# Kernel tuning notes

Measured on AMD Instinct MI355X. Metric: run time of the kernel, lower is better.

The kernel has to match this reference:

```python
import jax, jax.numpy as jnp
import numpy as np

N = 100000   # nodes
G = 256      # graphs
E = 120000   # edges per relation
IN = 162
HID = 128
R = 5
L = 2        # extra RGCN layers beyond the initial one


def setup_inputs() -> dict:
    key = jax.random.key(0)
    ks = jax.random.split(key, 24)
    s = 0.05
    inp = {
        "X": jax.random.normal(ks[0], (N, IN), jnp.float32),
        "batch": jnp.sort(jax.random.randint(ks[6], (N,), 0, G)),
    }
    for i in range(R):
        inp[f"edge_index{i+1}"] = jax.random.randint(ks[1 + i], (2, E), 0, N)
    # RGCN initial layer params
    inp["W0"] = jax.random.normal(ks[7], (R, IN, HID), jnp.float32) * s
    inp["root0"] = jax.random.normal(ks[8], (IN, HID), jnp.float32) * s
    inp["b0"] = jnp.zeros((HID,), jnp.float32)
    # stacked params for the L hidden RGCN layers
    inp["Wl"] = jax.random.normal(ks[9], (L, R, HID, HID), jnp.float32) * s
    inp["rootl"] = jax.random.normal(ks[10], (L, HID, HID), jnp.float32) * s
    inp["bl"] = jnp.zeros((L, HID), jnp.float32)
    # classification head
    inp["Wc1"] = jax.random.normal(ks[11], (HID, HID), jnp.float32) * s
    inp["bc1"] = jnp.zeros((HID,), jnp.float32)
    inp["Wc2"] = jax.random.normal(ks[12], (HID, HID), jnp.float32) * s
    inp["bc2"] = jnp.zeros((HID,), jnp.float32)
    inp["Wc3"] = jax.random.normal(ks[13], (HID, 1), jnp.float32) * s
    inp["bc3"] = jnp.zeros((1,), jnp.float32)
    return inp


def _seg_mean(msg, dst, num):
    # scatter-mean over destination nodes (PyG RGCNConv uses aggr='mean' per relation)
    s = jax.ops.segment_sum(msg, dst, num_segments=num)
    c = jax.ops.segment_sum(jnp.ones(msg.shape[0], msg.dtype), dst, num_segments=num)
    return s / jnp.maximum(c, 1.0)[:, None]


def _rgcn(x, W, root, b, src, dst):
    # src, dst: [R, E]; W: [R, d_in, d_out]
    msgs = jnp.einsum("ref,rfh->reh", x[src], W)          # [R, E, HID]
    agg = jax.vmap(_seg_mean, in_axes=(0, 0, None))(msgs, dst, N)  # [R, N, HID]
    return x @ root + b + agg.sum(0)


def reference(X, edge_index1, edge_index2, edge_index3, edge_index4, edge_index5,
              batch, W0, root0, b0, Wl, rootl, bl, Wc1, bc1, Wc2, bc2, Wc3, bc3):
    ei = jnp.stack([edge_index1, edge_index2, edge_index3, edge_index4, edge_index5])  # [R,2,E]
    src, dst = ei[:, 0, :], ei[:, 1, :]
    h = jax.nn.relu(_rgcn(X, W0, root0, b0, src, dst))
    for l in range(L):
        h = jax.nn.relu(_rgcn(h, Wl[l], rootl[l], bl[l], src, dst))
    # mean readout over graphs
    s = jax.ops.segment_sum(h, batch, num_segments=G)
    c = jax.ops.segment_sum(jnp.ones((N,), h.dtype), batch, num_segments=G)
    read = s / jnp.maximum(c, 1.0)[:, None]
    h = jax.nn.relu(read @ Wc1 + bc1)
    h = jax.nn.relu(h @ Wc2 + bc2)
    return h @ Wc3 + bc3
```

## Files before the change

### kernel.cpp

```cpp
#include <hip/hip_runtime.h>

#define N_NODES 100000
#define NPAD    100096
#define G_GRAPHS 256
#define IN_F 162
#define KPAD0 192
#define HID 128
#define R_REL 5
#define L_LAYERS 2
#define M5 (R_REL * N_NODES)

typedef __attribute__((ext_vector_type(8))) short bf16x8;
typedef __attribute__((ext_vector_type(4))) float f32x4;

__device__ __forceinline__ short f2bf(float f) {
    union { float f; unsigned u; } v; v.f = f;
    unsigned r = (v.u + 0x7fffu + ((v.u >> 16) & 1u)) >> 16;
    return (short)r;
}
__device__ __forceinline__ float bf2f(unsigned short u) {
    union { unsigned u; float f; } v; v.u = ((unsigned)u) << 16;
    return v.f;
}

__global__ void k_count(const int* e0, const int* e1, const int* e2,
                        const int* e3, const int* e4, int* cnt, int E) {
    int gid = blockIdx.x * 256 + threadIdx.x;
    if (gid >= R_REL * E) return;
    int r = gid / E, e = gid - r * E;
    const int* ei = (r == 0) ? e0 : (r == 1) ? e1 : (r == 2) ? e2 : (r == 3) ? e3 : e4;
    atomicAdd(&cnt[r * N_NODES + ei[E + e]], 1);
}

__global__ __launch_bounds__(256) void k_scan1(const int* __restrict__ cnt,
                                               int* __restrict__ off, int* __restrict__ bsum) {
    __shared__ int ts[256];
    int t = threadIdx.x;
    int base = blockIdx.x * 1024 + t * 4;
    int v[4];
    #pragma unroll
    for (int j = 0; j < 4; j++) {
        int d = base + j;
        int s = 0;
        if (d < N_NODES) {
            #pragma unroll
            for (int r = 0; r < R_REL; r++) s += cnt[r * N_NODES + d];
        }
        v[j] = s;
    }
    int tsum = v[0] + v[1] + v[2] + v[3];
    ts[t] = tsum; __syncthreads();
    for (int o = 1; o < 256; o <<= 1) {
        int x = (t >= o) ? ts[t - o] : 0;
        __syncthreads();
        ts[t] += x;
        __syncthreads();
    }
    if (t == 255) bsum[blockIdx.x] = ts[255];
    int run = ts[t] - tsum;
    #pragma unroll
    for (int j = 0; j < 4; j++) { if (base + j < N_NODES) off[base + j] = run; run += v[j]; }
}

__global__ __launch_bounds__(512) void k_scan2(int* bsum, int nblk) {
    __shared__ int ts[512];
    int t = threadIdx.x;
    int v = (t < nblk) ? bsum[t] : 0;
    ts[t] = v; __syncthreads();
    for (int o = 1; o < 512; o <<= 1) {
        int x = (t >= o) ? ts[t - o] : 0;
        __syncthreads();
        ts[t] += x;
        __syncthreads();
    }
    if (t < nblk) bsum[t] = ts[t] - v;
}

__global__ void k_scan3(const int* __restrict__ off, const int* __restrict__ bsum,
                        int* __restrict__ mstart, int* __restrict__ mcur,
                        const int* __restrict__ cnt, float* __restrict__ invc) {
    int i = blockIdx.x * 256 + threadIdx.x;
    if (i >= N_NODES) return;
    int o = off[i] + bsum[i >> 10];
    mstart[i] = o;
    mcur[i] = o;
    int tc = 0;
    #pragma unroll
    for (int r = 0; r < R_REL; r++) {
        int c = cnt[r * N_NODES + i];
        tc += c;
        invc[r * N_NODES + i] = 1.0f / (float)max(c, 1);
    }
    if (i == N_NODES - 1) mstart[N_NODES] = o + tc;
}

__global__ void k_fill(const int* e0, const int* e1, const int* e2,
                       const int* e3, const int* e4, int* mcur,
                       const float* __restrict__ invc,
                       int* __restrict__ mrec, float* __restrict__ mw, int E) {
    int gid = blockIdx.x * 256 + threadIdx.x;
    if (gid >= R_REL * E) return;
    int r = gid / E, e = gid - r * E;
    const int* ei = (r == 0) ? e0 : (r == 1) ? e1 : (r == 2) ? e2 : (r == 3) ? e3 : e4;
    int src = ei[e], dst = ei[E + e];
    int pos = atomicAdd(&mcur[dst], 1);
    mrec[pos] = ((1 + r) * NPAD + src) * HID;
    mw[pos] = invc[r * N_NODES + dst];
}

__global__ void k_tw0(const float* __restrict__ root0, const float* __restrict__ W0,
                      short* __restrict__ out) {
    int gid = blockIdx.x * 256 + threadIdx.x;
    if (gid >= 6 * 128 * KPAD0) return;
    int chunk = gid / (128 * KPAD0);
    int rem = gid - chunk * 128 * KPAD0;
    int col = rem / KPAD0;
    int k = rem - col * KPAD0;
    float v = 0.f;
    if (k < IN_F)
        v = (chunk == 0) ? root0[k * HID + col]
                         : W0[((size_t)(chunk - 1) * IN_F + k) * HID + col];
    out[gid] = f2bf(v);
}

__global__ void k_twl(const float* __restrict__ rootl, const float* __restrict__ Wl,
                      short* __restrict__ out) {
    int gid = blockIdx.x * 256 + threadIdx.x;
    if (gid >= L_LAYERS * 6 * 128 * HID) return;
    int l = gid / (6 * 128 * HID);
    int rem = gid - l * 6 * 128 * HID;
    int chunk = rem / (128 * HID);
    int rem2 = rem - chunk * 128 * HID;
    int col = rem2 / HID;
    int k = rem2 - col * HID;
    float v = (chunk == 0) ? rootl[((size_t)l * HID + k) * HID + col]
                           : Wl[(((size_t)l * R_REL + (chunk - 1)) * HID + k) * HID + col];
    out[gid] = f2bf(v);
}

template<int KP, bool A_F32>
__global__ __launch_bounds__(256, 2)
void gemm_fused(const void* __restrict__ Av, const short* __restrict__ Wt,
                unsigned short* __restrict__ Y, int M, int Kreal) {
    constexpr int SA = KP + 8;
    constexpr int NC8 = KP / 8;
    __shared__ short As[128 * SA];
    __shared__ short Bs[128 * SA];
    const int tid = threadIdx.x;
    const int row0 = blockIdx.x * 128;
    const int lane = tid & 63, wv = tid >> 6;
    const int quad = lane >> 4, l16 = lane & 15;
    const int wr0 = (wv >> 1) * 64, wc0 = (wv & 1) * 64;

    for (int cidx = tid; cidx < 128 * NC8; cidx += 256) {
        int row = cidx / NC8, c8 = cidx - row * NC8;
        int grow = row0 + row, k = c8 * 8;
        bf16x8 v = (bf16x8){0,0,0,0,0,0,0,0};
        if (grow < M) {
            if (A_F32) {
                const float* Af = (const float*)Av;
                #pragma unroll
                for (int j = 0; j < 8; j++) {
                    int kk = k + j;
                    float f = (kk < Kreal) ? Af[(size_t)grow * Kreal + kk] : 0.f;
                    v[j] = f2bf(f);
                }
            } else {
                v = *(const bf16x8*)((const short*)Av + (size_t)grow * KP + k);
            }
        }
        *(bf16x8*)&As[row * SA + k] = v;
    }

    for (int chunk = 0; chunk < 6; chunk++) {
        __syncthreads();
        const short* Wc = Wt + (size_t)chunk * 128 * KP;
        for (int cidx = tid; cidx < 128 * NC8; cidx += 256) {
            int row = cidx / NC8, c8 = cidx - row * NC8;
            *(bf16x8*)&Bs[row * SA + c8 * 8] = *(const bf16x8*)&Wc[row * KP + c8 * 8];
        }
        __syncthreads();

        f32x4 acc[4][4];
        #pragma unroll
        for (int i = 0; i < 4; i++)
            #pragma unroll
            for (int j = 0; j < 4; j++) acc[i][j] = (f32x4){0.f, 0.f, 0.f, 0.f};

        #pragma unroll
        for (int ks = 0; ks < KP / 32; ks++) {
            int k0 = ks * 32;
            bf16x8 af[4], bfr[4];
            #pragma unroll
            for (int i = 0; i < 4; i++)
                af[i] = *(const bf16x8*)&As[(wr0 + i * 16 + l16) * SA + k0 + quad * 8];
            #pragma unroll
            for (int j = 0; j < 4; j++)
                bfr[j] = *(const bf16x8*)&Bs[(wc0 + j * 16 + l16) * SA + k0 + quad * 8];
            #pragma unroll
            for (int i = 0; i < 4; i++)
                #pragma unroll
                for (int j = 0; j < 4; j++)
                    acc[i][j] = __builtin_amdgcn_mfma_f32_16x16x32_bf16(af[i], bfr[j], acc[i][j], 0, 0, 0);
        }
        __syncthreads();

        #pragma unroll
        for (int i = 0; i < 4; i++)
            #pragma unroll
            for (int j = 0; j < 4; j++)
                #pragma unroll
                for (int reg = 0; reg < 4; reg++)
                    Bs[(wr0 + i * 16 + quad * 4 + reg) * SA + wc0 + j * 16 + l16] =
                        f2bf(acc[i][j][reg]);
        __syncthreads();

        unsigned short* Yc = Y + (size_t)chunk * NPAD * HID + (size_t)row0 * HID;
        #pragma unroll
        for (int s = 0; s < 8; s++) {
            int row = (tid >> 4) + s * 16;
            int col = (tid & 15) * 8;
            bf16x8 v = *(const bf16x8*)&Bs[row * SA + col];
            *(bf16x8*)&Yc[(size_t)row * HID + col] = v;
        }
    }
}

__global__ __launch_bounds__(256)
void aggregate(const unsigned short* __restrict__ Yall, const int* __restrict__ mstart,
               const int* __restrict__ mrec, const float* __restrict__ mw,
               const float* __restrict__ bias, unsigned short* __restrict__ hout) {
    int wid = (blockIdx.x * 256 + threadIdx.x) >> 6;
    int lane = threadIdx.x & 63;
    if (wid >= N_NODES) return;
    int d = wid;
    int s = mstart[d], e = mstart[d + 1];

    float2 b2 = *(const float2*)&bias[lane * 2];
    unsigned rv = *(const unsigned*)&Yall[(size_t)d * HID + lane * 2];
    float s0 = b2.x + bf2f((unsigned short)(rv & 0xffff));
    float s1 = b2.y + bf2f((unsigned short)(rv >> 16));

    for (int base = s; base < e; base += 64) {
        int m = e - base;
        int rec = 0; float w = 0.f;
        if (lane < m) { rec = mrec[base + lane]; w = mw[base + lane]; }
        int cnt = min(m, 64);
        for (int j = 0; j < cnt; j++) {
            int off = __shfl(rec, j, 64);
            float wj = __shfl(w, j, 64);
            unsigned v = *(const unsigned*)&Yall[(size_t)off + lane * 2];
            s0 += wj * bf2f((unsigned short)(v & 0xffff));
            s1 += wj * bf2f((unsigned short)(v >> 16));
        }
    }
    unsigned lo = (unsigned short)f2bf(fmaxf(s0, 0.f));
    unsigned hi = (unsigned short)f2bf(fmaxf(s1, 0.f));
    *(unsigned*)&hout[(size_t)d * HID + lane * 2] = lo | (hi << 16);
}

__global__ __launch_bounds__(128)
void k_pool(const unsigned short* __restrict__ h, const int* __restrict__ batch,
            float* __restrict__ pooled) {
    int c = threadIdx.x;
    int start = blockIdx.x * 128;
    if (start >= N_NODES) return;
    int end = min(start + 128, N_NODES);
    int g = batch[start];
    float s = 0.f;
    for (int i = start; i < end; i++) {
        int gi = batch[i];
        if (gi != g) { atomicAdd(&pooled[g * HID + c], s); s = 0.f; g = gi; }
        s += bf2f(h[(size_t)i * HID + c]);
    }
    atomicAdd(&pooled[g * HID + c], s);
}

__device__ int lower_bound_i(const int* a, int n, int v) {
    int lo = 0, hi = n;
    while (lo < hi) {
        int mid = (lo + hi) >> 1;
        if (a[mid] < v) lo = mid + 1; else hi = mid;
    }
    return lo;
}

__global__ __launch_bounds__(128)
void k_mlp(const float* __restrict__ pooled, const int* __restrict__ batch,
           const float* __restrict__ Wc1, const float* __restrict__ bc1,
           const float* __restrict__ Wc2, const float* __restrict__ bc2,
           const float* __restrict__ Wc3, const float* __restrict__ bc3,
           float* __restrict__ out) {
    int g = blockIdx.x;
    int c = threadIdx.x;
    __shared__ int range[2];
    if (c == 0) range[0] = lower_bound_i(batch, N_NODES, g);
    if (c == 1) range[1] = lower_bound_i(batch, N_NODES, g + 1);
    __syncthreads();
    float denom = fmaxf((float)(range[1] - range[0]), 1.0f);
    __shared__ float row[HID], h1[HID], h2[HID];
    row[c] = pooled[g * HID + c] / denom;
    __syncthreads();
    float acc = bc1[c];
    for (int k = 0; k < HID; k++) acc += row[k] * Wc1[k * HID + c];
    h1[c] = fmaxf(acc, 0.f);
    __syncthreads();
    acc = bc2[c];
    for (int k = 0; k < HID; k++) acc += h1[k] * Wc2[k * HID + c];
    h2[c] = fmaxf(acc, 0.f);
    __syncthreads();
    float t = h2[c] * Wc3[c];
    for (int off = 32; off > 0; off >>= 1) t += __shfl_down(t, off, 64);
    __shared__ float part[2];
    if ((c & 63) == 0) part[c >> 6] = t;
    __syncthreads();
    if (c == 0) out[g] = part[0] + part[1] + bc3[0];
}

extern "C" void kernel_launch(void* const* d_in, const int* in_sizes, int n_in,
                              void* d_out, int out_size, void* d_ws, size_t ws_size,
                              hipStream_t stream) {
    const float* X     = (const float*)d_in[0];
    const int*   batch = (const int*)d_in[1];
    const int*   e0 = (const int*)d_in[2];
    const int*   e1 = (const int*)d_in[3];
    const int*   e2 = (const int*)d_in[4];
    const int*   e3 = (const int*)d_in[5];
    const int*   e4 = (const int*)d_in[6];
    const float* W0    = (const float*)d_in[7];
    const float* root0 = (const float*)d_in[8];
    const float* b0    = (const float*)d_in[9];
    const float* Wl    = (const float*)d_in[10];
    const float* rootl = (const float*)d_in[11];
    const float* bl    = (const float*)d_in[12];
    const float* Wc1   = (const float*)d_in[13];
    const float* bc1   = (const float*)d_in[14];
    const float* Wc2   = (const float*)d_in[15];
    const float* bc2   = (const float*)d_in[16];
    const float* Wc3   = (const float*)d_in[17];
    const float* bc3   = (const float*)d_in[18];
    const int E = in_sizes[2] / 2;
    const int NE = R_REL * E;

    char* base = (char*)d_ws;
    size_t o = 0;
    auto carve = [&](size_t bytes) -> char* {
        char* p = base + o;
        o = (o + bytes + 255) & ~(size_t)255;
        return p;
    };
    unsigned short* Y    = (unsigned short*)carve((size_t)6 * NPAD * HID * 2);
    unsigned short* hA   = (unsigned short*)carve((size_t)NPAD * HID * 2);
    unsigned short* hB   = (unsigned short*)carve((size_t)NPAD * HID * 2);
    int*   cnt    = (int*)carve((size_t)M5 * 4);
    float* invc   = (float*)carve((size_t)M5 * 4);
    int*   offsc  = (int*)carve((size_t)N_NODES * 4);
    int*   mstart = (int*)carve((size_t)(N_NODES + 1) * 4);
    int*   mcur   = (int*)carve((size_t)N_NODES * 4);
    int*   mrec   = (int*)carve((size_t)NE * 4);
    float* mw     = (float*)carve((size_t)NE * 4);
    int*   bsum   = (int*)carve(2048);
    float* pooled = (float*)carve((size_t)G_GRAPHS * HID * 4);
    short* Wt0    = (short*)carve((size_t)6 * 128 * KPAD0 * 2);
    short* Wtl    = (short*)carve((size_t)L_LAYERS * 6 * 128 * HID * 2);

    hipMemsetAsync(cnt, 0, (size_t)M5 * 4, stream);
    hipMemsetAsync(pooled, 0, (size_t)G_GRAPHS * HID * 4, stream);
    int eg = (NE + 255) / 256;
    k_count<<<eg, 256, 0, stream>>>(e0, e1, e2, e3, e4, cnt, E);
    int nblk = (N_NODES + 1023) / 1024;
    k_scan1<<<nblk, 256, 0, stream>>>(cnt, offsc, bsum);
    k_scan2<<<1, 512, 0, stream>>>(bsum, nblk);
    k_scan3<<<(N_NODES + 255) / 256, 256, 0, stream>>>(offsc, bsum, mstart, mcur, cnt, invc);
    k_fill<<<eg, 256, 0, stream>>>(e0, e1, e2, e3, e4, mcur, invc, mrec, mw, E);

    k_tw0<<<(6 * 128 * KPAD0 + 255) / 256, 256, 0, stream>>>(root0, W0, Wt0);
    k_twl<<<(L_LAYERS * 6 * 128 * HID + 255) / 256, 256, 0, stream>>>(rootl, Wl, Wtl);

    int ggrid = NPAD / 128;
    int agg_grid = (N_NODES + 3) / 4;

    gemm_fused<KPAD0, true><<<ggrid, 256, 0, stream>>>(X, Wt0, Y, N_NODES, IN_F);
    aggregate<<<agg_grid, 256, 0, stream>>>(Y, mstart, mrec, mw, b0, hA);

    unsigned short* hin = hA; unsigned short* hout = hB;
    for (int l = 0; l < L_LAYERS; l++) {
        gemm_fused<HID, false><<<ggrid, 256, 0, stream>>>(hin, Wtl + (size_t)l * 6 * 128 * HID,
                                                          Y, N_NODES, HID);
        aggregate<<<agg_grid, 256, 0, stream>>>(Y, mstart, mrec, mw, bl + (size_t)l * HID, hout);
        unsigned short* t = hin; hin = hout; hout = t;
    }

    k_pool<<<(N_NODES + 127) / 128, 128, 0, stream>>>(hin, batch, pooled);
    k_mlp<<<G_GRAPHS, 128, 0, stream>>>(pooled, batch, Wc1, bc1, Wc2, bc2, Wc3, bc3, (float*)d_out);
}
```

Measured before the change: 718.8 us.

## Split GEMM across output chunks with direct register A loads and XCD-aware tiling

Replaces the GEMM that staged the A tile in LDS and looped over six weight chunks inside one block. Each block now computes a single chunk, so the grid is six times larger, and it reads A fragments straight from global memory into registers with prefetching. Block IDs are remapped so the row tiles that share A land on the same XCD, aiming for L2 reuse. X is pre-cast to padded bf16 by a new kernel. The cost is reading A six times from global or L2 memory plus an extra cast pass over X.

```diff
diff --git a/kernel.cpp b/kernel.cpp
--- a/kernel.cpp
+++ b/kernel.cpp
@@ -2,6 +2,8 @@
 
 #define N_NODES 100000
 #define NPAD    100096
+#define NTILES  782
+#define TPX     98
 #define G_GRAPHS 256
 #define IN_F 162
 #define KPAD0 192
@@ -106,6 +108,14 @@
     int pos = atomicAdd(&mcur[dst], 1);
     mrec[pos] = ((1 + r) * NPAD + src) * HID;
     mw[pos] = invc[r * N_NODES + dst];
+}
+
+__global__ void k_castX(const float* __restrict__ X, unsigned short* __restrict__ Xb) {
+    int gid = blockIdx.x * 256 + threadIdx.x;
+    if (gid >= NPAD * KPAD0) return;
+    int row = gid / KPAD0, k = gid - row * KPAD0;
+    float v = (row < N_NODES && k < IN_F) ? X[(size_t)row * IN_F + k] : 0.f;
+    Xb[gid] = (unsigned short)f2bf(v);
 }
 
 __global__ void k_tw0(const float* __restrict__ root0, const float* __restrict__ W0,
@@ -138,62 +148,61 @@
     out[gid] = f2bf(v);
 }
 
-template<int KP, bool A_F32>
-__global__ __launch_bounds__(256, 2)
-void gemm_fused(const void* __restrict__ Av, const short* __restrict__ Wt,
-                unsigned short* __restrict__ Y, int M, int Kreal) {
+template<int KP>
+__global__ __launch_bounds__(256)
+void gemm_direct(const unsigned short* __restrict__ A, const short* __restrict__ Wt,
+                 unsigned short* __restrict__ Y) {
+    constexpr int KS = KP / 32;
+    constexpr int PF = (KS > 4) ? 2 : KS;
     constexpr int SA = KP + 8;
-    constexpr int NC8 = KP / 8;
-    __shared__ short As[128 * SA];
     __shared__ short Bs[128 * SA];
+
+    int bid = blockIdx.x;
+    int xcd = bid & 7, slot = bid >> 3;
+    int chunk = slot / TPX;
+    int rt = xcd * TPX + (slot - chunk * TPX);
+    if (rt >= NTILES) return;
+    const int row0 = rt * 128;
+
     const int tid = threadIdx.x;
-    const int row0 = blockIdx.x * 128;
     const int lane = tid & 63, wv = tid >> 6;
     const int quad = lane >> 4, l16 = lane & 15;
     const int wr0 = (wv >> 1) * 64, wc0 = (wv & 1) * 64;
 
-    for (int cidx = tid; cidx < 128 * NC8; cidx += 256) {
-        int row = cidx / NC8, c8 = cidx - row * NC8;
-        int grow = row0 + row, k = c8 * 8;
-        bf16x8 v = (bf16x8){0,0,0,0,0,0,0,0};
-        if (grow < M) {
-            if (A_F32) {
-                const float* Af = (const float*)Av;
-                #pragma unroll
-                for (int j = 0; j < 8; j++) {
-                    int kk = k + j;
-                    float f = (kk < Kreal) ? Af[(size_t)grow * Kreal + kk] : 0.f;
-                    v[j] = f2bf(f);
-                }
-            } else {
-                v = *(const bf16x8*)((const short*)Av + (size_t)grow * KP + k);
-            }
-        }
-        *(bf16x8*)&As[row * SA + k] = v;
-    }
-
-    for (int chunk = 0; chunk < 6; chunk++) {
-        __syncthreads();
-        const short* Wc = Wt + (size_t)chunk * 128 * KP;
-        for (int cidx = tid; cidx < 128 * NC8; cidx += 256) {
-            int row = cidx / NC8, c8 = cidx - row * NC8;
-            *(bf16x8*)&Bs[row * SA + c8 * 8] = *(const bf16x8*)&Wc[row * KP + c8 * 8];
-        }
-        __syncthreads();
-
-        f32x4 acc[4][4];
+    const size_t arow = (size_t)(row0 + wr0 + l16) * KP + quad * 8;
+
+    bf16x8 cur[PF][4], nxt[PF][4];
+    #pragma unroll
+    for (int p = 0; p < PF; p++)
         #pragma unroll
         for (int i = 0; i < 4; i++)
-            #pragma unroll
-            for (int j = 0; j < 4; j++) acc[i][j] = (f32x4){0.f, 0.f, 0.f, 0.f};
-
+            cur[p][i] = *(const bf16x8*)&A[arow + (size_t)i * 16 * KP + p * 32];
+
+    const short* Wc = Wt + (size_t)chunk * 128 * KP;
+    for (int cidx = tid; cidx < 128 * (KP / 8); cidx += 256) {
+        int row = cidx / (KP / 8), c8 = cidx - row * (KP / 8);
+        *(bf16x8*)&Bs[row * SA + c8 * 8] = *(const bf16x8*)&Wc[row * KP + c8 * 8];
+    }
+    __syncthreads();
+
+    f32x4 acc[4][4];
+    #pragma unroll
+    for (int i = 0; i < 4; i++)
         #pragma unroll
-        for (int ks = 0; ks < KP / 32; ks++) {
-            int k0 = ks * 32;
-            bf16x8 af[4], bfr[4];
-            #pragma unroll
-            for (int i = 0; i < 4; i++)
-                af[i] = *(const bf16x8*)&As[(wr0 + i * 16 + l16) * SA + k0 + quad * 8];
+        for (int j = 0; j < 4; j++) acc[i][j] = (f32x4){0.f, 0.f, 0.f, 0.f};
+
+    for (int kb = 0; kb < KS; kb += PF) {
+        if (kb + PF < KS) {
+            #pragma unroll
+            for (int p = 0; p < PF; p++)
+                #pragma unroll
+                for (int i = 0; i < 4; i++)
+                    nxt[p][i] = *(const bf16x8*)&A[arow + (size_t)i * 16 * KP + (kb + PF + p) * 32];
+        }
+        #pragma unroll
+        for (int p = 0; p < PF; p++) {
+            int k0 = (kb + p) * 32;
+            bf16x8 bfr[4];
             #pragma unroll
             for (int j = 0; j < 4; j++)
                 bfr[j] = *(const bf16x8*)&Bs[(wc0 + j * 16 + l16) * SA + k0 + quad * 8];
@@ -201,28 +210,33 @@
             for (int i = 0; i < 4; i++)
                 #pragma unroll
                 for (int j = 0; j < 4; j++)
-                    acc[i][j] = __builtin_amdgcn_mfma_f32_16x16x32_bf16(af[i], bfr[j], acc[i][j], 0, 0, 0);
+                    acc[i][j] = __builtin_amdgcn_mfma_f32_16x16x32_bf16(cur[p][i], bfr[j], acc[i][j], 0, 0, 0);
         }
-        __syncthreads();
-
         #pragma unroll
-        for (int i = 0; i < 4; i++)
-            #pragma unroll
-            for (int j = 0; j < 4; j++)
-                #pragma unroll
-                for (int reg = 0; reg < 4; reg++)
-                    Bs[(wr0 + i * 16 + quad * 4 + reg) * SA + wc0 + j * 16 + l16] =
-                        f2bf(acc[i][j][reg]);
-        __syncthreads();
-
-        unsigned short* Yc = Y + (size_t)chunk * NPAD * HID + (size_t)row0 * HID;
+        for (int p = 0; p < PF; p++)
+            #pragma unroll
+            for (int i = 0; i < 4; i++)
+                cur[p][i] = nxt[p][i];
+    }
+    __syncthreads();
+
+    #pragma unroll
+    for (int i = 0; i < 4; i++)
         #pragma unroll
-        for (int s = 0; s < 8; s++) {
-            int row = (tid >> 4) + s * 16;
-            int col = (tid & 15) * 8;
-            bf16x8 v = *(const bf16x8*)&Bs[row * SA + col];
-            *(bf16x8*)&Yc[(size_t)row * HID + col] = v;
-        }
+        for (int j = 0; j < 4; j++)
+            #pragma unroll
+            for (int reg = 0; reg < 4; reg++)
+                Bs[(wr0 + i * 16 + quad * 4 + reg) * SA + wc0 + j * 16 + l16] =
+                    f2bf(acc[i][j][reg]);
+    __syncthreads();
+
+    unsigned short* Yc = Y + (size_t)chunk * NPAD * HID + (size_t)row0 * HID;
+    #pragma unroll
+    for (int s = 0; s < 8; s++) {
+        int row = (tid >> 4) + s * 16;
+        int col = (tid & 15) * 8;
+        bf16x8 v = *(const bf16x8*)&Bs[row * SA + col];
+        *(bf16x8*)&Yc[(size_t)row * HID + col] = v;
     }
 }
 
@@ -352,6 +366,7 @@
     unsigned short* Y    = (unsigned short*)carve((size_t)6 * NPAD * HID * 2);
     unsigned short* hA   = (unsigned short*)carve((size_t)NPAD * HID * 2);
     unsigned short* hB   = (unsigned short*)carve((size_t)NPAD * HID * 2);
+    unsigned short* Xb   = (unsigned short*)carve((size_t)NPAD * KPAD0 * 2);
     int*   cnt    = (int*)carve((size_t)M5 * 4);
     float* invc   = (float*)carve((size_t)M5 * 4);
     int*   offsc  = (int*)carve((size_t)N_NODES * 4);
@@ -373,20 +388,19 @@
     k_scan2<<<1, 512, 0, stream>>>(bsum, nblk);
     k_scan3<<<(N_NODES + 255) / 256, 256, 0, stream>>>(offsc, bsum, mstart, mcur, cnt, invc);
     k_fill<<<eg, 256, 0, stream>>>(e0, e1, e2, e3, e4, mcur, invc, mrec, mw, E);
-
+    k_castX<<<(NPAD * KPAD0 + 255) / 256, 256, 0, stream>>>(X, Xb);
     k_tw0<<<(6 * 128 * KPAD0 + 255) / 256, 256, 0, stream>>>(root0, W0, Wt0);
     k_twl<<<(L_LAYERS * 6 * 128 * HID + 255) / 256, 256, 0, stream>>>(rootl, Wl, Wtl);
 
-    int ggrid = NPAD / 128;
+    int ggrid = 8 * TPX * 6;
     int agg_grid = (N_NODES + 3) / 4;
 
-    gemm_fused<KPAD0, true><<<ggrid, 256, 0, stream>>>(X, Wt0, Y, N_NODES, IN_F);
+    gemm_direct<KPAD0><<<ggrid, 256, 0, stream>>>(Xb, Wt0, Y);
     aggregate<<<agg_grid, 256, 0, stream>>>(Y, mstart, mrec, mw, b0, hA);
 
     unsigned short* hin = hA; unsigned short* hout = hB;
     for (int l = 0; l < L_LAYERS; l++) {
-        gemm_fused<HID, false><<<ggrid, 256, 0, stream>>>(hin, Wtl + (size_t)l * 6 * 128 * HID,
-                                                          Y, N_NODES, HID);
+        gemm_direct<HID><<<ggrid, 256, 0, stream>>>(hin, Wtl + (size_t)l * 6 * 128 * HID, Y);
         aggregate<<<agg_grid, 256, 0, stream>>>(Y, mstart, mrec, mw, bl + (size_t)l * HID, hout);
         unsigned short* t = hin; hin = hout; hout = t;
     }
```

Measured after the change: 693.3 us. -3.5%, faster.

## Keep GEMM A-tile in registers and batch gather loads in aggregate

Applied to the files above, without the earlier changes.

The GEMM kernel no longer stages the A tile in shared memory. Each wave loads its A fragments straight from global memory into registers once and reuses them across all six weight chunks, which cuts LDS use and raises occupancy for the hidden layers. The aggregate kernel now issues up to eight independent gather loads before accumulating, so more memory requests are in flight. The trade-off is higher register pressure: the first layer holds 24 bf16x8 fragments per thread. The A loads are also uncoalesced direct fragment loads.

```diff
diff --git a/kernel.cpp b/kernel.cpp
--- a/kernel.cpp
+++ b/kernel.cpp
@@ -2,6 +2,7 @@
 
 #define N_NODES 100000
 #define NPAD    100096
+#define NTILES  782
 #define G_GRAPHS 256
 #define IN_F 162
 #define KPAD0 192
@@ -138,46 +139,62 @@
     out[gid] = f2bf(v);
 }
 
-template<int KP, bool A_F32>
-__global__ __launch_bounds__(256, 2)
-void gemm_fused(const void* __restrict__ Av, const short* __restrict__ Wt,
-                unsigned short* __restrict__ Y, int M, int Kreal) {
-    constexpr int SA = KP + 8;
-    constexpr int NC8 = KP / 8;
-    __shared__ short As[128 * SA];
-    __shared__ short Bs[128 * SA];
+template<int SEG, bool A_F32, int MINW>
+__global__ __launch_bounds__(256, MINW)
+void gemm_reg(const void* __restrict__ Av, const short* __restrict__ Wt,
+              unsigned short* __restrict__ Y) {
+    constexpr int KSEG = SEG / 32;
+    constexpr int SBP = SEG + 8;
+    __shared__ short Bs[128 * SBP];
     const int tid = threadIdx.x;
     const int row0 = blockIdx.x * 128;
     const int lane = tid & 63, wv = tid >> 6;
     const int quad = lane >> 4, l16 = lane & 15;
     const int wr0 = (wv >> 1) * 64, wc0 = (wv & 1) * 64;
 
-    for (int cidx = tid; cidx < 128 * NC8; cidx += 256) {
-        int row = cidx / NC8, c8 = cidx - row * NC8;
-        int grow = row0 + row, k = c8 * 8;
-        bf16x8 v = (bf16x8){0,0,0,0,0,0,0,0};
-        if (grow < M) {
-            if (A_F32) {
-                const float* Af = (const float*)Av;
-                #pragma unroll
-                for (int j = 0; j < 8; j++) {
-                    int kk = k + j;
-                    float f = (kk < Kreal) ? Af[(size_t)grow * Kreal + kk] : 0.f;
-                    v[j] = f2bf(f);
+    bf16x8 af[KSEG][4];
+    #pragma unroll
+    for (int i = 0; i < 4; i++) {
+        int grow = row0 + wr0 + i * 16 + l16;
+        if (A_F32) {
+            const float* rp = (const float*)Av + (size_t)grow * IN_F;
+            bool ok = grow < N_NODES;
+            #pragma unroll
+            for (int kb = 0; kb < KSEG; kb++) {
+                bf16x8 v;
+                if (kb < 5) {
+                    int k = kb * 32 + quad * 8;
+                    #pragma unroll
+                    for (int h = 0; h < 4; h++) {
+                        float2 f2 = ok ? *(const float2*)(rp + k + 2 * h)
+                                       : make_float2(0.f, 0.f);
+                        v[2 * h] = f2bf(f2.x); v[2 * h + 1] = f2bf(f2.y);
+                    }
+                } else {
+                    int k = 160 + quad * 8;
+                    #pragma unroll
+                    for (int j = 0; j < 8; j++) {
+                        int kk = k + j;
+                        float f = (ok && kk < IN_F) ? rp[kk] : 0.f;
+                        v[j] = f2bf(f);
+                    }
                 }
-            } else {
-                v = *(const bf16x8*)((const short*)Av + (size_t)grow * KP + k);
+                af[kb][i] = v;
             }
-        }
-        *(bf16x8*)&As[row * SA + k] = v;
+        } else {
+            const unsigned short* Ab = (const unsigned short*)Av;
+            #pragma unroll
+            for (int kb = 0; kb < KSEG; kb++)
+                af[kb][i] = *(const bf16x8*)&Ab[(size_t)grow * SEG + kb * 32 + quad * 8];
+        }
     }
 
     for (int chunk = 0; chunk < 6; chunk++) {
-        __syncthreads();
-        const short* Wc = Wt + (size_t)chunk * 128 * KP;
-        for (int cidx = tid; cidx < 128 * NC8; cidx += 256) {
-            int row = cidx / NC8, c8 = cidx - row * NC8;
-            *(bf16x8*)&Bs[row * SA + c8 * 8] = *(const bf16x8*)&Wc[row * KP + c8 * 8];
+        if (chunk) __syncthreads();
+        const short* Wc = Wt + (size_t)chunk * 128 * SEG;
+        for (int c = tid; c < 128 * (SEG / 8); c += 256) {
+            int r = c / (SEG / 8), c8 = (c - r * (SEG / 8)) * 8;
+            *(bf16x8*)&Bs[r * SBP + c8] = *(const bf16x8*)&Wc[r * SEG + c8];
         }
         __syncthreads();
 
@@ -188,20 +205,16 @@
             for (int j = 0; j < 4; j++) acc[i][j] = (f32x4){0.f, 0.f, 0.f, 0.f};
 
         #pragma unroll
-        for (int ks = 0; ks < KP / 32; ks++) {
-            int k0 = ks * 32;
-            bf16x8 af[4], bfr[4];
-            #pragma unroll
-            for (int i = 0; i < 4; i++)
-                af[i] = *(const bf16x8*)&As[(wr0 + i * 16 + l16) * SA + k0 + quad * 8];
+        for (int kb = 0; kb < KSEG; kb++) {
+            bf16x8 bfr[4];
             #pragma unroll
             for (int j = 0; j < 4; j++)
-                bfr[j] = *(const bf16x8*)&Bs[(wc0 + j * 16 + l16) * SA + k0 + quad * 8];
+                bfr[j] = *(const bf16x8*)&Bs[(wc0 + j * 16 + l16) * SBP + kb * 32 + quad * 8];
             #pragma unroll
             for (int i = 0; i < 4; i++)
                 #pragma unroll
                 for (int j = 0; j < 4; j++)
-                    acc[i][j] = __builtin_amdgcn_mfma_f32_16x16x32_bf16(af[i], bfr[j], acc[i][j], 0, 0, 0);
+                    acc[i][j] = __builtin_amdgcn_mfma_f32_16x16x32_bf16(af[kb][i], bfr[j], acc[i][j], 0, 0, 0);
         }
         __syncthreads();
 
@@ -211,7 +224,7 @@
             for (int j = 0; j < 4; j++)
                 #pragma unroll
                 for (int reg = 0; reg < 4; reg++)
-                    Bs[(wr0 + i * 16 + quad * 4 + reg) * SA + wc0 + j * 16 + l16] =
+                    Bs[(wr0 + i * 16 + quad * 4 + reg) * SBP + wc0 + j * 16 + l16] =
                         f2bf(acc[i][j][reg]);
         __syncthreads();
 
@@ -220,7 +233,7 @@
         for (int s = 0; s < 8; s++) {
             int row = (tid >> 4) + s * 16;
             int col = (tid & 15) * 8;
-            bf16x8 v = *(const bf16x8*)&Bs[row * SA + col];
+            bf16x8 v = *(const bf16x8*)&Bs[row * SBP + col];
             *(bf16x8*)&Yc[(size_t)row * HID + col] = v;
         }
     }
@@ -242,16 +255,25 @@
     float s1 = b2.y + bf2f((unsigned short)(rv >> 16));
 
     for (int base = s; base < e; base += 64) {
-        int m = e - base;
+        int m = min(e - base, 64);
         int rec = 0; float w = 0.f;
         if (lane < m) { rec = mrec[base + lane]; w = mw[base + lane]; }
-        int cnt = min(m, 64);
-        for (int j = 0; j < cnt; j++) {
-            int off = __shfl(rec, j, 64);
-            float wj = __shfl(w, j, 64);
-            unsigned v = *(const unsigned*)&Yall[(size_t)off + lane * 2];
-            s0 += wj * bf2f((unsigned short)(v & 0xffff));
-            s1 += wj * bf2f((unsigned short)(v >> 16));
+        for (int j = 0; j < m; j += 8) {
+            int g = min(8, m - j);
+            unsigned v[8]; float wj[8];
+            #pragma unroll
+            for (int t = 0; t < 8; t++) {
+                if (t < g) {
+                    int off = __shfl(rec, j + t, 64);
+                    wj[t] = __shfl(w, j + t, 64);
+                    v[t] = *(const unsigned*)&Yall[(size_t)off + lane * 2];
+                } else { v[t] = 0u; wj[t] = 0.f; }
+            }
+            #pragma unroll
+            for (int t = 0; t < 8; t++) {
+                s0 += wj[t] * bf2f((unsigned short)(v[t] & 0xffff));
+                s1 += wj[t] * bf2f((unsigned short)(v[t] >> 16));
+            }
         }
     }
     unsigned lo = (unsigned short)f2bf(fmaxf(s0, 0.f));
@@ -373,20 +395,17 @@
     k_scan2<<<1, 512, 0, stream>>>(bsum, nblk);
     k_scan3<<<(N_NODES + 255) / 256, 256, 0, stream>>>(offsc, bsum, mstart, mcur, cnt, invc);
     k_fill<<<eg, 256, 0, stream>>>(e0, e1, e2, e3, e4, mcur, invc, mrec, mw, E);
-
     k_tw0<<<(6 * 128 * KPAD0 + 255) / 256, 256, 0, stream>>>(root0, W0, Wt0);
     k_twl<<<(L_LAYERS * 6 * 128 * HID + 255) / 256, 256, 0, stream>>>(rootl, Wl, Wtl);
 
-    int ggrid = NPAD / 128;
     int agg_grid = (N_NODES + 3) / 4;
 
-    gemm_fused<KPAD0, true><<<ggrid, 256, 0, stream>>>(X, Wt0, Y, N_NODES, IN_F);
+    gemm_reg<KPAD0, true, 2><<<NTILES, 256, 0, stream>>>(X, Wt0, Y);
     aggregate<<<agg_grid, 256, 0, stream>>>(Y, mstart, mrec, mw, b0, hA);
 
     unsigned short* hin = hA; unsigned short* hout = hB;
     for (int l = 0; l < L_LAYERS; l++) {
-        gemm_fused<HID, false><<<ggrid, 256, 0, stream>>>(hin, Wtl + (size_t)l * 6 * 128 * HID,
-                                                          Y, N_NODES, HID);
+        gemm_reg<HID, false, 3><<<NTILES, 256, 0, stream>>>(hin, Wtl + (size_t)l * 6 * 128 * HID, Y);
         aggregate<<<agg_grid, 256, 0, stream>>>(Y, mstart, mrec, mw, bl + (size_t)l * HID, hout);
         unsigned short* t = hin; hin = hout; hout = t;
     }
```

Measured after the change: 738.7 us. +2.8%, slower.
